# Kernel optimization log

Measured on AMD Instinct MI355X. Metric: run time of the kernel, lower is better.

## Reference

```python
import jax, jax.numpy as jnp
import numpy as np

VOCAB, EDIM, ENC, H, OUT = 50000, 128, 128, 100, 104
B, L, NPT = 128, 64, 64          # batch, statements per seq, nodes per statement tree
N = B * L * NPT                  # 524288 total nodes
MAXD = 6                         # max depth of a 64-node complete binary tree


def setup_inputs() -> dict:
    key = jax.random.key(0)
    ks = jax.random.split(key, 14)
    tokens = jax.random.randint(ks[0], (N,), 0, VOCAB)
    # structured tree topology: each statement tree is a 64-node complete binary tree
    local = np.arange(NPT)
    par_local = np.where(local == 0, 0, (local - 1) // 2)
    depth_local = np.floor(np.log2(local + 1)).astype(np.int32)
    base = np.repeat(np.arange(B * L) * NPT, NPT)
    parent = jnp.asarray(base + np.tile(par_local, B * L), dtype=jnp.int32)
    depth = jnp.asarray(np.tile(depth_local, B * L), dtype=jnp.int32)
    tree_id = jnp.asarray(np.repeat(np.arange(B * L), NPT), dtype=jnp.int32)
    nrm = lambda k, s, sc: jax.random.normal(k, s, jnp.float32) * sc
    return {
        "tokens": tokens, "parent": parent, "depth": depth, "tree_id": tree_id,
        "emb": nrm(ks[1], (VOCAB, EDIM), 0.02),
        "W_lin": nrm(ks[2], (ENC, EDIM), 0.05), "b_lin": nrm(ks[3], (ENC,), 0.05),
        "Wi_f": nrm(ks[4], (3 * H, ENC), 0.05), "Wh_f": nrm(ks[5], (3 * H, H), 0.05),
        "bi_f": nrm(ks[6], (3 * H,), 0.05), "bh_f": nrm(ks[7], (3 * H,), 0.05),
        "Wi_b": nrm(ks[8], (3 * H, ENC), 0.05), "Wh_b": nrm(ks[9], (3 * H, H), 0.05),
        "bi_b": nrm(ks[10], (3 * H,), 0.05), "bh_b": nrm(ks[11], (3 * H,), 0.05),
        "W_fc": nrm(ks[12], (OUT, 2 * H), 0.05), "b_fc": nrm(ks[13], (OUT,), 0.05),
    }


def _gru_scan(x_seq, Wi, Wh, bi, bh):
    # x_seq: [L, B, ENC] -> outputs [L, B, H]. Matches torch.nn.GRU cell math.
    def step(hprev, xt):
        gi = xt @ Wi.T + bi              # [B, 3H]
        gh = hprev @ Wh.T + bh
        ir, iz, inn = jnp.split(gi, 3, axis=-1)
        hr, hz, hn = jnp.split(gh, 3, axis=-1)
        r = jax.nn.sigmoid(ir + hr)
        z = jax.nn.sigmoid(iz + hz)
        n = jnp.tanh(inn + r * hn)
        hnew = (1.0 - z) * n + z * hprev
        return hnew, hnew
    h0 = jnp.zeros((x_seq.shape[1], Wh.shape[1]), x_seq.dtype)
    _, ys = jax.lax.scan(step, h0, x_seq)
    return ys


def reference(tokens, parent, depth, tree_id, emb, W_lin, b_lin,
              Wi_f, Wh_f, bi_f, bh_f, Wi_b, Wh_b, bi_b, bh_b, W_fc, b_fc):
    # per-node value: linear(embedding(token))   [N, ENC]
    h = emb[tokens] @ W_lin.T + b_lin
    # bottom-up subtree sum: h(node) = v(node) + sum(h(children)), batched by depth level
    for d in range(MAXD, 0, -1):
        contrib = jnp.where((depth == d)[:, None], h, 0.0)
        h = h.at[parent].add(contrib)
    # TreeEncoder output: max over all node hidden states of each tree
    encodes = jax.ops.segment_max(h, tree_id, num_segments=B * L)  # [B*L, ENC]
    x = encodes.reshape(B, L, ENC).transpose(1, 0, 2)              # [L, B, ENC]
    yf = _gru_scan(x, Wi_f, Wh_f, bi_f, bh_f)                      # [L, B, H]
    yb = _gru_scan(x[::-1], Wi_b, Wh_b, bi_b, bh_b)[::-1]
    gru_out = jnp.concatenate([yf, yb], axis=-1)                   # [L, B, 2H]
    pooled = gru_out.max(axis=0)                                   # [B, 2H]
    return pooled @ W_fc.T + b_fc                                  # [B, OUT]
```

## Files before the change

kernel.cpp:

```cpp
#include <hip/hip_runtime.h>
#include <hip/hip_bf16.h>

typedef __bf16 bf16_t;
typedef __attribute__((ext_vector_type(8))) __bf16 bf16x8;
typedef __attribute__((ext_vector_type(4))) float f32x4;

#define TREES 8192
#define ENC 128
#define HH 100
#define G3 300
#define GSTRIDE 304
#define BB 128
#define LL 64
#define OUTD 104
#define TPB_TREES 8

__device__ __forceinline__ float sigm(float x) { return 1.0f / (1.0f + __expf(-x)); }
__device__ __forceinline__ float tanh_f(float x) { return 2.0f / (1.0f + __expf(-2.0f * x)) - 1.0f; }
__device__ __forceinline__ float bflo(unsigned int u) { return __builtin_bit_cast(float, u << 16); }
__device__ __forceinline__ float bfhi(unsigned int u) { return __builtin_bit_cast(float, u & 0xffff0000u); }

__device__ __forceinline__ int subtree_size(int n) {
  int np1 = n + 1;
  int d = 31 - __clz(np1);
  return ((64 >> d) - 1) + (((np1 & (np1 - 1)) == 0) ? 1 : 0);
}

__global__ __launch_bounds__(256) void k0_prep(const float* __restrict__ W_lin,
                                               const float* __restrict__ Wi_f,
                                               const float* __restrict__ Wi_b,
                                               const float* __restrict__ emb,
                                               bf16_t* __restrict__ Wbf,
                                               bf16_t* __restrict__ Wibf,
                                               bf16_t* __restrict__ embbf) {
  int i = blockIdx.x * 256 + threadIdx.x;
  if (i < 1600000) {
    float4 v = ((const float4*)emb)[i];
    ushort4 u;
    u.x = __builtin_bit_cast(unsigned short, (bf16_t)v.x);
    u.y = __builtin_bit_cast(unsigned short, (bf16_t)v.y);
    u.z = __builtin_bit_cast(unsigned short, (bf16_t)v.z);
    u.w = __builtin_bit_cast(unsigned short, (bf16_t)v.w);
    ((ushort4*)embbf)[i] = u;
  }
  if (i < 128 * 128) Wbf[i] = (bf16_t)W_lin[i];
  if (i < 608 * 128) {
    int jg = i >> 7, k = i & 127;
    int dir = (jg >= GSTRIDE) ? 1 : 0;
    int j = jg - dir * GSTRIDE;
    float v = 0.0f;
    if (j < G3) v = dir ? Wi_b[j * 128 + k] : Wi_f[j * 128 + k];
    Wibf[i] = (bf16_t)v;
  }
}

__global__ __launch_bounds__(256) void k1_tree(const int* __restrict__ tokens,
                                               const bf16_t* __restrict__ embbf,
                                               const bf16_t* __restrict__ Wbf,
                                               const float* __restrict__ b_lin,
                                               float* __restrict__ encodes) {
  __shared__ float s[64][132];
  __shared__ float maxbuf[2][128];
  __shared__ float sb[128];
  int tid = threadIdx.x;
  int wave = tid >> 6;
  int lane = tid & 63;
  int ri = lane & 15;
  int kg = lane >> 4;
  int wm = wave >> 1;
  int wn = wave & 1;

  if (tid < 128) sb[tid] = b_lin[tid];

  bf16x8 bfr[4][4];
#pragma unroll
  for (int ks = 0; ks < 4; ++ks)
#pragma unroll
    for (int ni = 0; ni < 4; ++ni)
      bfr[ks][ni] = *(const bf16x8*)(Wbf + (size_t)((wn * 4 + ni) * 16 + ri) * 128 +
                                     ks * 32 + kg * 8);

  float szs[2][4];
#pragma unroll
  for (int mi = 0; mi < 2; ++mi)
#pragma unroll
    for (int rr = 0; rr < 4; ++rr)
      szs[mi][rr] = (float)subtree_size(wm * 32 + mi * 16 + kg * 4 + rr);

  int n = tid >> 2;
  int q = tid & 3;
  int tree0 = blockIdx.x * TPB_TREES;

  uint4 pre[4];
  {
    int tok = tokens[tree0 * 64 + n];
    const uint4* src = (const uint4*)(embbf + (size_t)tok * ENC) + q * 4;
#pragma unroll
    for (int i = 0; i < 4; ++i) pre[i] = src[i];
  }

  for (int t = 0; t < TPB_TREES; ++t) {
    int tree = tree0 + t;

#pragma unroll
    for (int i = 0; i < 4; ++i) {
      uint4 p = pre[i];
      float4 f0 = {bflo(p.x), bfhi(p.x), bflo(p.y), bfhi(p.y)};
      float4 f1 = {bflo(p.z), bfhi(p.z), bflo(p.w), bfhi(p.w)};
      *(float4*)&s[n][q * 32 + i * 8] = f0;
      *(float4*)&s[n][q * 32 + i * 8 + 4] = f1;
    }
    __syncthreads();

    if (t + 1 < TPB_TREES) {
      int tok = tokens[(tree + 1) * 64 + n];
      const uint4* src = (const uint4*)(embbf + (size_t)tok * ENC) + q * 4;
#pragma unroll
      for (int i = 0; i < 4; ++i) pre[i] = src[i];
    }

    if (tid < 128) s[31][tid] += s[63][tid];
    __syncthreads();
    for (int lev = 4; lev >= 0; --lev) {
      int p0 = (1 << lev) - 1;
      int items = (1 << lev) * 128;
      for (int it = tid; it < items; it += 256) {
        int p = p0 + (it >> 7);
        int c = it & 127;
        s[p][c] += s[2 * p + 1][c] + s[2 * p + 2][c];
      }
      __syncthreads();
    }

    f32x4 acc[2][4];
#pragma unroll
    for (int mi = 0; mi < 2; ++mi)
#pragma unroll
      for (int ni = 0; ni < 4; ++ni) {
        f32x4 z = {0.f, 0.f, 0.f, 0.f};
        acc[mi][ni] = z;
      }
#pragma unroll
    for (int ks = 0; ks < 4; ++ks) {
      int k0 = ks * 32 + kg * 8;
#pragma unroll
      for (int mi = 0; mi < 2; ++mi) {
        float4 a0 = *(const float4*)&s[wm * 32 + mi * 16 + ri][k0];
        float4 a1 = *(const float4*)&s[wm * 32 + mi * 16 + ri][k0 + 4];
        bf16x8 afr;
        afr[0] = (bf16_t)a0.x; afr[1] = (bf16_t)a0.y; afr[2] = (bf16_t)a0.z; afr[3] = (bf16_t)a0.w;
        afr[4] = (bf16_t)a1.x; afr[5] = (bf16_t)a1.y; afr[6] = (bf16_t)a1.z; afr[7] = (bf16_t)a1.w;
#pragma unroll
        for (int ni = 0; ni < 4; ++ni)
          acc[mi][ni] = __builtin_amdgcn_mfma_f32_16x16x32_bf16(afr, bfr[ks][ni], acc[mi][ni], 0, 0, 0);
      }
    }

    float cmax[4];
#pragma unroll
    for (int ni = 0; ni < 4; ++ni) {
      float bl = sb[(wn * 4 + ni) * 16 + ri];
      float m = -1e30f;
#pragma unroll
      for (int mi = 0; mi < 2; ++mi) {
        f32x4 a = acc[mi][ni];
        m = fmaxf(m, fmaxf(fmaxf(a.x + szs[mi][0] * bl, a.y + szs[mi][1] * bl),
                           fmaxf(a.z + szs[mi][2] * bl, a.w + szs[mi][3] * bl)));
      }
      cmax[ni] = m;
    }
#pragma unroll
    for (int off = 16; off < 64; off <<= 1) {
#pragma unroll
      for (int ni = 0; ni < 4; ++ni)
        cmax[ni] = fmaxf(cmax[ni], __shfl_xor(cmax[ni], off));
    }
    if (lane < 16) {
#pragma unroll
      for (int ni = 0; ni < 4; ++ni) maxbuf[wm][(wn * 4 + ni) * 16 + lane] = cmax[ni];
    }
    __syncthreads();
    if (tid < 128) {
      encodes[(size_t)tree * ENC + tid] = fmaxf(maxbuf[0][tid], maxbuf[1][tid]);
    }
    __syncthreads();
  }
}

__global__ __launch_bounds__(256) void k2_gi(const float* __restrict__ encodes,
                                             const bf16_t* __restrict__ Wibf,
                                             const float* __restrict__ bi_f,
                                             const float* __restrict__ bi_b,
                                             float* __restrict__ GI) {
  int tid = threadIdx.x;
  int wave = tid >> 6;
  int lane = tid & 63;
  int ri = lane & 15;
  int kg = lane >> 4;
  int m0 = blockIdx.x * 16;

  f32x4 acc[10];
#pragma unroll
  for (int i = 0; i < 10; ++i) {
    f32x4 z = {0.f, 0.f, 0.f, 0.f};
    acc[i] = z;
  }

  int r = m0 + ri;
  int er = (r & 127) * 64 + (r >> 7);
  const float* arow = encodes + (size_t)er * ENC;
#pragma unroll
  for (int ks = 0; ks < 4; ++ks) {
    int k0 = ks * 32 + kg * 8;
    float4 a0 = *(const float4*)(arow + k0);
    float4 a1 = *(const float4*)(arow + k0 + 4);
    bf16x8 afr;
    afr[0] = (bf16_t)a0.x; afr[1] = (bf16_t)a0.y; afr[2] = (bf16_t)a0.z; afr[3] = (bf16_t)a0.w;
    afr[4] = (bf16_t)a1.x; afr[5] = (bf16_t)a1.y; afr[6] = (bf16_t)a1.z; afr[7] = (bf16_t)a1.w;
#pragma unroll
    for (int i = 0; i < 10; ++i) {
      int nt = wave + i * 4;
      if (nt < 38) {
        bf16x8 bfr = *(const bf16x8*)(Wibf + (nt * 16 + ri) * 128 + k0);
        acc[i] = __builtin_amdgcn_mfma_f32_16x16x32_bf16(afr, bfr, acc[i], 0, 0, 0);
      }
    }
  }
#pragma unroll
  for (int i = 0; i < 10; ++i) {
    int nt = wave + i * 4;
    if (nt >= 38) continue;
    int jg = nt * 16 + ri;
    int dir = (jg >= GSTRIDE) ? 1 : 0;
    int j = jg - dir * GSTRIDE;
    if (j >= G3) continue;
    float bias = dir ? bi_b[j] : bi_f[j];
#pragma unroll
    for (int rr = 0; rr < 4; ++rr) {
      int rowg = m0 + kg * 4 + rr;
      int l = rowg >> 7, b = rowg & 127;
      GI[(((size_t)dir * LL + l) * BB + b) * GSTRIDE + j] = acc[i][rr] + bias;
    }
  }
}

__global__ __launch_bounds__(640) void k3_gru(const float* __restrict__ GI,
                                              const float* __restrict__ Wh_f,
                                              const float* __restrict__ Wh_b,
                                              const float* __restrict__ bh_f,
                                              const float* __restrict__ bh_b,
                                              float* __restrict__ pooled) {
  int blk = blockIdx.x;
  int dir = blk >> 7;
  int b = blk & 127;
  int tid = threadIdx.x;
  __shared__ __align__(16) float h_lds[104];
  __shared__ float gh_lds[304];
  __shared__ float gi_lds[2][304];
  const float* Wh = dir ? Wh_b : Wh_f;
  const float* bh = dir ? bh_b : bh_f;

  int j = tid >> 1;
  int kg = tid & 1;
  int kbase = kg * 52;
  bool isdot = (tid < 600);

  float4 wv[13];
  float bhj = 0.f;
  if (isdot) {
#pragma unroll
    for (int c = 0; c < 13; ++c) {
      int k0 = kbase + c * 4;
      float4 v;
      v.x = (k0 + 0 < HH) ? Wh[j * HH + k0 + 0] : 0.f;
      v.y = (k0 + 1 < HH) ? Wh[j * HH + k0 + 1] : 0.f;
      v.z = (k0 + 2 < HH) ? Wh[j * HH + k0 + 2] : 0.f;
      v.w = (k0 + 3 < HH) ? Wh[j * HH + k0 + 3] : 0.f;
      wv[c] = v;
    }
    if (kg == 0) bhj = bh[j];
  }
  if (tid < 104) h_lds[tid] = 0.f;

  const float* giB = GI + (size_t)dir * LL * BB * GSTRIDE + (size_t)b * GSTRIDE;
  if (tid < G3) {
    int la0 = dir ? 63 : 0;
    gi_lds[0][tid] = giB[(size_t)la0 * BB * GSTRIDE + tid];
  }
  float ymax = -1e30f;
  __syncthreads();

  for (int step = 0; step < 64; ++step) {
    int cur = step & 1;
    int nxt = cur ^ 1;
    float ginext = 0.f;
    if (tid < G3) {
      int ns = (step < 63) ? step + 1 : 63;
      int la = dir ? (63 - ns) : ns;
      ginext = giB[(size_t)la * BB * GSTRIDE + tid];
    }
    if (isdot) {
      float a0 = 0.f, a1 = 0.f, a2 = 0.f, a3 = 0.f;
#pragma unroll
      for (int c = 0; c < 13; ++c) {
        float4 hv = *(const float4*)&h_lds[kbase + c * 4];
        a0 += wv[c].x * hv.x;
        a1 += wv[c].y * hv.y;
        a2 += wv[c].z * hv.z;
        a3 += wv[c].w * hv.w;
      }
      float p = (a0 + a1) + (a2 + a3);
      p += __shfl_xor(p, 1);
      if (kg == 0) gh_lds[j] = p + bhj;
    }
    __syncthreads();
    if (tid < HH) {
      float r = sigm(gi_lds[cur][tid] + gh_lds[tid]);
      float z = sigm(gi_lds[cur][100 + tid] + gh_lds[100 + tid]);
      float n = tanh_f(gi_lds[cur][200 + tid] + r * gh_lds[200 + tid]);
      float hnew = (1.f - z) * n + z * h_lds[tid];
      ymax = fmaxf(ymax, hnew);
      h_lds[tid] = hnew;
    }
    if (tid < G3 && step < 63) gi_lds[nxt][tid] = ginext;
    __syncthreads();
  }
  if (tid < HH) pooled[(size_t)b * 200 + dir * 100 + tid] = ymax;
}

__global__ __launch_bounds__(128) void k4_fc(const float* __restrict__ pooled,
                                             const float* __restrict__ W_fc,
                                             const float* __restrict__ b_fc,
                                             float* __restrict__ out) {
  int b = blockIdx.x;
  int o = threadIdx.x;
  if (o >= OUTD) return;
  const float* p = pooled + (size_t)b * 200;
  const float* w = W_fc + (size_t)o * 200;
  float acc = b_fc[o];
#pragma unroll 8
  for (int j = 0; j < 200; ++j) acc += p[j] * w[j];
  out[(size_t)b * OUTD + o] = acc;
}

extern "C" void kernel_launch(void* const* d_in, const int* in_sizes, int n_in,
                              void* d_out, int out_size, void* d_ws, size_t ws_size,
                              hipStream_t stream) {
  const int* tokens = (const int*)d_in[0];
  const float* emb = (const float*)d_in[4];
  const float* W_lin = (const float*)d_in[5];
  const float* b_lin = (const float*)d_in[6];
  const float* Wi_f = (const float*)d_in[7];
  const float* Wh_f = (const float*)d_in[8];
  const float* bi_f = (const float*)d_in[9];
  const float* bh_f = (const float*)d_in[10];
  const float* Wi_b = (const float*)d_in[11];
  const float* Wh_b = (const float*)d_in[12];
  const float* bi_b = (const float*)d_in[13];
  const float* bh_b = (const float*)d_in[14];
  const float* W_fc = (const float*)d_in[15];
  const float* b_fc = (const float*)d_in[16];

  float* encodes = (float*)d_ws;
  float* GI = encodes + (size_t)TREES * ENC;
  float* pooled = GI + (size_t)2 * LL * BB * GSTRIDE;
  bf16_t* Wbf = (bf16_t*)(pooled + (size_t)BB * 200);
  bf16_t* Wibf = Wbf + 128 * 128;
  bf16_t* embbf = (bf16_t*)GI;

  k0_prep<<<6250, 256, 0, stream>>>(W_lin, Wi_f, Wi_b, emb, Wbf, Wibf, embbf);
  k1_tree<<<TREES / TPB_TREES, 256, 0, stream>>>(tokens, embbf, Wbf, b_lin, encodes);
  k2_gi<<<512, 256, 0, stream>>>(encodes, Wibf, bi_f, bi_b, GI);
  k3_gru<<<256, 640, 0, stream>>>(GI, Wh_f, Wh_b, bh_f, bh_b, pooled);
  k4_fc<<<BB, 128, 0, stream>>>(pooled, W_fc, b_fc, (float*)d_out);
}
```

Baseline: 160.1 us.

## Restructure tree subtree-sum into per-column register reduction with fewer barriers

The level-by-level subtree sum in the tree kernel, which needed a block barrier per level, is replaced. Now each pair of threads owns one column and carries partial sums in registers through levels 4..0, combining the two halves with a lane shuffle. The shared tile padding changes from 132 to 129 with an XOR-style column swizzle applied to the writes, the reduction and the MFMA A-fragment reads, to cut LDS bank conflicts. Barriers become a lightweight waitcnt+s_barrier, and the trailing per-tree barrier is dropped. A stride of 129 floats leaves 16-byte vector LDS accesses misaligned on odd rows, which may cost performance or rely on unaligned LDS support.

```diff
diff --git a/kernel.cpp b/kernel.cpp
--- a/kernel.cpp
+++ b/kernel.cpp
@@ -19,6 +19,10 @@
 __device__ __forceinline__ float tanh_f(float x) { return 2.0f / (1.0f + __expf(-2.0f * x)) - 1.0f; }
 __device__ __forceinline__ float bflo(unsigned int u) { return __builtin_bit_cast(float, u << 16); }
 __device__ __forceinline__ float bfhi(unsigned int u) { return __builtin_bit_cast(float, u & 0xffff0000u); }
+
+__device__ __forceinline__ void ldsbar() {
+  asm volatile("s_waitcnt lgkmcnt(0)\n\ts_barrier" ::: "memory");
+}
 
 __device__ __forceinline__ int subtree_size(int n) {
   int np1 = n + 1;
@@ -59,7 +63,7 @@
                                                const bf16_t* __restrict__ Wbf,
                                                const float* __restrict__ b_lin,
                                                float* __restrict__ encodes) {
-  __shared__ float s[64][132];
+  __shared__ float s_[64][129];
   __shared__ float maxbuf[2][128];
   __shared__ float sb[128];
   int tid = threadIdx.x;
@@ -89,6 +93,9 @@
 
   int n = tid >> 2;
   int q = tid & 3;
+  int c = tid >> 1;
+  int half = tid & 1;
+  int pc = (c & ~31) | ((((c >> 3) + (c >> 5)) & 3) << 3) | (c & 7);
   int tree0 = blockIdx.x * TPB_TREES;
 
   uint4 pre[4];
@@ -98,6 +105,7 @@
 #pragma unroll
     for (int i = 0; i < 4; ++i) pre[i] = src[i];
   }
+  __syncthreads();
 
   for (int t = 0; t < TPB_TREES; ++t) {
     int tree = tree0 + t;
@@ -107,10 +115,10 @@
       uint4 p = pre[i];
       float4 f0 = {bflo(p.x), bfhi(p.x), bflo(p.y), bfhi(p.y)};
       float4 f1 = {bflo(p.z), bfhi(p.z), bflo(p.w), bfhi(p.w)};
-      *(float4*)&s[n][q * 32 + i * 8] = f0;
-      *(float4*)&s[n][q * 32 + i * 8 + 4] = f1;
-    }
-    __syncthreads();
+      int col = q * 32 + (((i + q) & 3) << 3);
+      *(float4*)&s_[n][col] = f0;
+      *(float4*)&s_[n][col + 4] = f1;
+    }
 
     if (t + 1 < TPB_TREES) {
       int tok = tokens[(tree + 1) * 64 + n];
@@ -118,19 +126,41 @@
 #pragma unroll
       for (int i = 0; i < 4; ++i) pre[i] = src[i];
     }
-
-    if (tid < 128) s[31][tid] += s[63][tid];
-    __syncthreads();
-    for (int lev = 4; lev >= 0; --lev) {
-      int p0 = (1 << lev) - 1;
-      int items = (1 << lev) * 128;
-      for (int it = tid; it < items; it += 256) {
-        int p = p0 + (it >> 7);
-        int c = it & 127;
-        s[p][c] += s[2 * p + 1][c] + s[2 * p + 2][c];
-      }
-      __syncthreads();
-    }
+    ldsbar();
+
+    if (half == 0) s_[31][pc] += s_[63][pc];
+    {
+      float r[8];
+      int pb = 15 + half * 8;
+#pragma unroll
+      for (int i = 0; i < 8; ++i) {
+        int p = pb + i;
+        r[i] = s_[p][pc] + s_[2 * p + 1][pc] + s_[2 * p + 2][pc];
+        s_[p][pc] = r[i];
+      }
+      float tt[4];
+      int pb2 = 7 + half * 4;
+#pragma unroll
+      for (int i = 0; i < 4; ++i) {
+        int p = pb2 + i;
+        tt[i] = s_[p][pc] + r[2 * i] + r[2 * i + 1];
+        s_[p][pc] = tt[i];
+      }
+      float uu[2];
+      int pb3 = 3 + half * 2;
+#pragma unroll
+      for (int i = 0; i < 2; ++i) {
+        int p = pb3 + i;
+        uu[i] = s_[p][pc] + tt[2 * i] + tt[2 * i + 1];
+        s_[p][pc] = uu[i];
+      }
+      int p1 = 1 + half;
+      float w1 = s_[p1][pc] + uu[0] + uu[1];
+      s_[p1][pc] = w1;
+      float w2 = __shfl_xor(w1, 1);
+      if (half == 0) s_[0][pc] = s_[0][pc] + w1 + w2;
+    }
+    ldsbar();
 
     f32x4 acc[2][4];
 #pragma unroll
@@ -142,11 +172,12 @@
       }
 #pragma unroll
     for (int ks = 0; ks < 4; ++ks) {
-      int k0 = ks * 32 + kg * 8;
+      int k0p = ks * 32 + (((kg + ks) & 3) << 3);
 #pragma unroll
       for (int mi = 0; mi < 2; ++mi) {
-        float4 a0 = *(const float4*)&s[wm * 32 + mi * 16 + ri][k0];
-        float4 a1 = *(const float4*)&s[wm * 32 + mi * 16 + ri][k0 + 4];
+        int row = wm * 32 + mi * 16 + ri;
+        float4 a0 = *(const float4*)&s_[row][k0p];
+        float4 a1 = *(const float4*)&s_[row][k0p + 4];
         bf16x8 afr;
         afr[0] = (bf16_t)a0.x; afr[1] = (bf16_t)a0.y; afr[2] = (bf16_t)a0.z; afr[3] = (bf16_t)a0.w;
         afr[4] = (bf16_t)a1.x; afr[5] = (bf16_t)a1.y; afr[6] = (bf16_t)a1.z; afr[7] = (bf16_t)a1.w;
@@ -179,11 +210,10 @@
 #pragma unroll
       for (int ni = 0; ni < 4; ++ni) maxbuf[wm][(wn * 4 + ni) * 16 + lane] = cmax[ni];
     }
-    __syncthreads();
+    ldsbar();
     if (tid < 128) {
       encodes[(size_t)tree * ENC + tid] = fmaxf(maxbuf[0][tid], maxbuf[1][tid]);
     }
-    __syncthreads();
   }
 }
 
```

Measured after the change: 142.2 us. -11.2%, faster.
